# Kernel tuning notes

Hardware: AMD Instinct MI355X
Metric: run time of the kernel (lower is better)

## Reference

```python
import jax, jax.numpy as jnp
import numpy as np

BLOCK_LEN = 64

def _segsum(x):
    """x: (..., T) -> (..., T, T) with segment sums on/below diagonal, -inf above."""
    T = x.shape[-1]
    cs = jnp.cumsum(x, axis=-1)
    seg = cs[..., :, None] - cs[..., None, :]
    mask = jnp.tril(jnp.ones((T, T), dtype=bool))
    return jnp.where(mask, seg, -jnp.inf)

def setup_inputs() -> dict:
    key = jax.random.key(0)
    kX, kA, kB, kC = jax.random.split(key, 4)
    B, S, H, P, N = 2, 4096, 32, 64, 64
    X = jax.random.normal(kX, (B, S, H, P), dtype=jnp.float32)
    # negative decay rates keep exp(cumsum) bounded (real Mamba2 uses A<0)
    A = -jnp.abs(jax.random.normal(kA, (B, S, H), dtype=jnp.float32)) * 0.1
    Bm = jax.random.normal(kB, (B, S, H, N), dtype=jnp.float32)
    Cm = jax.random.normal(kC, (B, S, H, N), dtype=jnp.float32)
    return {"X": X, "A": A, "Bm": Bm, "Cm": Cm}

def reference(X, A, Bm, Cm):
    b, s, h, p = X.shape
    n = Bm.shape[-1]
    l = BLOCK_LEN
    c = s // l
    Xb = X.reshape(b, c, l, h, p)
    Bb = Bm.reshape(b, c, l, h, n)
    Cb = Cm.reshape(b, c, l, h, n)
    Ab = A.reshape(b, c, l, h).transpose(0, 3, 1, 2)  # (b,h,c,l)

    # intra-chunk decay matrix L = exp(segsum(A))  (b,h,c,l,l)
    L = jnp.exp(_segsum(Ab))
    Y_diag = jnp.einsum('bclhn,bcshn,bhcls,bcshp->bclhp', Cb, Bb, L, Xb)

    A_cumsum = jnp.cumsum(Ab, axis=-1)  # (b,h,c,l)
    decay_states = jnp.exp(A_cumsum[..., :, -1:] - A_cumsum)
    states = jnp.einsum('bclhn,bhcl,bclhp->bchpn', Bb, decay_states, Xb)

    init = jnp.zeros_like(states[:, :1])
    states = jnp.concatenate([init, states], axis=1)  # (b,c+1,h,p,n)

    chunk_last = jnp.pad(A_cumsum[..., -1], ((0, 0), (0, 0), (1, 0)))  # (b,h,c+1)
    decay_chunk = jnp.exp(_segsum(chunk_last))  # (b,h,c+1,c+1)
    new_states = jnp.einsum('bhzc,bchpn->bzhpn', decay_chunk, states)
    states = new_states[:, :-1]  # (b,c,h,p,n)

    state_decay_out = jnp.exp(A_cumsum)
    Y_off = jnp.einsum('bclhn,bchpn,bhcl->bclhp', Cb, states, state_decay_out)

    Y = (Y_diag + Y_off).reshape(b, s, h, p)
    return Y
```

## Files before the change

### kernel.cpp

```cpp
#include <hip/hip_runtime.h>
#include <hip/hip_bf16.h>

#define B_ 2
#define S_ 4096
#define H_ 32
#define P_ 64
#define N_ 64
#define C_ 64
#define HP 2048
#define HN 2048

__device__ __forceinline__ float bf2f(unsigned int u16) {
    return __uint_as_float(u16 << 16);
}
__device__ __forceinline__ void unpack2(unsigned int u, float& lo, float& hi) {
    lo = __uint_as_float(u << 16);
    hi = __uint_as_float(u & 0xffff0000u);
}
__device__ __forceinline__ unsigned short f2bf(float f) {
    unsigned int u = __float_as_uint(f);
    u += 0x7fffu + ((u >> 16) & 1u);
    return (unsigned short)(u >> 16);
}

__global__ void k0_detect(const unsigned short* __restrict__ Au, int* __restrict__ flag)
{
    int tid = threadIdx.x;
    unsigned short u = Au[tid * 2];
    int positive = ((u & 0x8000u) == 0) ? 1 : 0;
    unsigned long long m = __ballot(positive);
    if (tid == 0) *flag = (__popcll(m) > 8) ? 1 : 0;
}

__global__ __launch_bounds__(256) void k1_states(
    const void* __restrict__ Xg,
    const void* __restrict__ Ag,
    const void* __restrict__ Bg,
    float* __restrict__ states,
    float* __restrict__ sums,
    const int* __restrict__ flag)
{
    __shared__ __align__(16) float Xs[64][68];
    __shared__ __align__(16) float BwT[64][68];
    __shared__ float wdec[64];

    const int tid = threadIdx.x;
    const int bid = blockIdx.x;
    const int h = bid & 31;
    const int c = (bid >> 5) & 63;
    const int b = bid >> 11;
    const int isf32 = *flag;

    if (tid < 64) {
        int ai = (b * S_ + c * 64 + tid) * H_ + h;
        float a = isf32 ? ((const float*)Ag)[ai] : bf2f(((const unsigned short*)Ag)[ai]);
        float x = a;
        #pragma unroll
        for (int off = 1; off < 64; off <<= 1) {
            float y = __shfl_up(x, off, 64);
            if (tid >= off) x += y;
        }
        float tot = __shfl(x, 63, 64);
        wdec[tid] = __expf(tot - x);
        if (tid == 63) sums[(b * H_ + h) * C_ + c] = tot;
    }
    __syncthreads();

    const size_t baseX = (size_t)((b * S_ + c * 64) * H_ + h) * P_;
    const size_t baseB = (size_t)((b * S_ + c * 64) * H_ + h) * N_;

    if (!isf32) {
        const unsigned short* Xp = (const unsigned short*)Xg + baseX;
        const unsigned short* Bp = (const unsigned short*)Bg + baseB;
        #pragma unroll
        for (int it = 0; it < 2; ++it) {
            int f = it * 2048 + tid * 8;
            int t = f >> 6;
            int e = f & 63;
            uint4 rx = *(const uint4*)(Xp + (size_t)t * HP + e);
            float v0,v1,v2,v3,v4,v5,v6,v7;
            unpack2(rx.x, v0, v1); unpack2(rx.y, v2, v3);
            unpack2(rx.z, v4, v5); unpack2(rx.w, v6, v7);
            float* xr = &Xs[t][e];
            xr[0]=v0; xr[1]=v1; xr[2]=v2; xr[3]=v3; xr[4]=v4; xr[5]=v5; xr[6]=v6; xr[7]=v7;

            uint4 rb = *(const uint4*)(Bp + (size_t)t * HN + e);
            float w = wdec[t];
            unpack2(rb.x, v0, v1); unpack2(rb.y, v2, v3);
            unpack2(rb.z, v4, v5); unpack2(rb.w, v6, v7);
            BwT[e+0][t]=v0*w; BwT[e+1][t]=v1*w; BwT[e+2][t]=v2*w; BwT[e+3][t]=v3*w;
            BwT[e+4][t]=v4*w; BwT[e+5][t]=v5*w; BwT[e+6][t]=v6*w; BwT[e+7][t]=v7*w;
        }
    } else {
        const float* Xp = (const float*)Xg + baseX;
        const float* Bp = (const float*)Bg + baseB;
        #pragma unroll
        for (int it = 0; it < 2; ++it) {
            int f = it * 2048 + tid * 8;
            int t = f >> 6;
            int e = f & 63;
            float4 x0 = *(const float4*)(Xp + (size_t)t * HP + e);
            float4 x1 = *(const float4*)(Xp + (size_t)t * HP + e + 4);
            float* xr = &Xs[t][e];
            xr[0]=x0.x; xr[1]=x0.y; xr[2]=x0.z; xr[3]=x0.w;
            xr[4]=x1.x; xr[5]=x1.y; xr[6]=x1.z; xr[7]=x1.w;

            float4 b0 = *(const float4*)(Bp + (size_t)t * HN + e);
            float4 b1 = *(const float4*)(Bp + (size_t)t * HN + e + 4);
            float w = wdec[t];
            BwT[e+0][t]=b0.x*w; BwT[e+1][t]=b0.y*w; BwT[e+2][t]=b0.z*w; BwT[e+3][t]=b0.w*w;
            BwT[e+4][t]=b1.x*w; BwT[e+5][t]=b1.y*w; BwT[e+6][t]=b1.z*w; BwT[e+7][t]=b1.w*w;
        }
    }
    __syncthreads();

    const int tr = tid >> 4, tc = tid & 15;
    float acc[4][4];
    #pragma unroll
    for (int i = 0; i < 4; ++i)
        #pragma unroll
        for (int j = 0; j < 4; ++j) acc[i][j] = 0.f;

    #pragma unroll 4
    for (int k4 = 0; k4 < 16; ++k4) {
        float la[4][4];
        #pragma unroll
        for (int i = 0; i < 4; ++i) {
            float4 v = *(const float4*)&BwT[tr * 4 + i][k4 * 4];
            la[i][0]=v.x; la[i][1]=v.y; la[i][2]=v.z; la[i][3]=v.w;
        }
        #pragma unroll
        for (int kk = 0; kk < 4; ++kk) {
            float4 r = *(const float4*)&Xs[k4 * 4 + kk][tc * 4];
            #pragma unroll
            for (int i = 0; i < 4; ++i) {
                acc[i][0] += la[i][kk] * r.x;
                acc[i][1] += la[i][kk] * r.y;
                acc[i][2] += la[i][kk] * r.z;
                acc[i][3] += la[i][kk] * r.w;
            }
        }
    }

    float* sp = states + (size_t)((b * C_ + c) * H_ + h) * 4096;
    #pragma unroll
    for (int i = 0; i < 4; ++i) {
        float4 v; v.x=acc[i][0]; v.y=acc[i][1]; v.z=acc[i][2]; v.w=acc[i][3];
        *(float4*)&sp[(tr * 4 + i) * 64 + tc * 4] = v;
    }
}

__global__ __launch_bounds__(256) void k2_scan(
    float* __restrict__ states, const float* __restrict__ sums)
{
    const int tid = threadIdx.x;
    const int bid = blockIdx.x;
    const int split = bid & 3;
    const int bh = bid >> 2;
    const int h = bh & 31;
    const int b = bh >> 5;
    const int e = split * 1024 + tid * 4;
    const float* sm = sums + (b * H_ + h) * C_;
    float4 S; S.x=0.f; S.y=0.f; S.z=0.f; S.w=0.f;
    for (int c = 0; c < 64; ++c) {
        float* p = states + (size_t)((b * C_ + c) * H_ + h) * 4096 + e;
        float4 st = *(const float4*)p;
        *(float4*)p = S;
        float d = __expf(sm[c]);
        S.x = S.x * d + st.x;
        S.y = S.y * d + st.y;
        S.z = S.z * d + st.z;
        S.w = S.w * d + st.w;
    }
}

__global__ __launch_bounds__(256) void k3_y(
    const void* __restrict__ Xg,
    const void* __restrict__ Ag,
    const void* __restrict__ Bg,
    const void* __restrict__ Cg,
    const float* __restrict__ states,
    void* __restrict__ Yg,
    const int* __restrict__ flag)
{
    __shared__ __align__(16) float Cs[64][68];
    __shared__ __align__(16) float Mb[64][68];
    __shared__ __align__(16) float Rb[64][68];
    __shared__ float cs[64];

    const int tid = threadIdx.x;
    const int bid = blockIdx.x;
    const int h = bid & 31;
    const int c = (bid >> 5) & 63;
    const int b = bid >> 11;
    const int isf32 = *flag;

    if (tid < 64) {
        int ai = (b * S_ + c * 64 + tid) * H_ + h;
        float a = isf32 ? ((const float*)Ag)[ai] : bf2f(((const unsigned short*)Ag)[ai]);
        float x = a;
        #pragma unroll
        for (int off = 1; off < 64; off <<= 1) {
            float y = __shfl_up(x, off, 64);
            if (tid >= off) x += y;
        }
        cs[tid] = x;
    }

    const size_t baseX = (size_t)((b * S_ + c * 64) * H_ + h) * P_;
    const size_t baseN = (size_t)((b * S_ + c * 64) * H_ + h) * N_;

    if (!isf32) {
        const unsigned short* Bp = (const unsigned short*)Bg + baseN;
        const unsigned short* Cp = (const unsigned short*)Cg + baseN;
        #pragma unroll
        for (int it = 0; it < 2; ++it) {
            int f = it * 2048 + tid * 8;
            int t = f >> 6;
            int e = f & 63;
            uint4 rc = *(const uint4*)(Cp + (size_t)t * HN + e);
            float v0,v1,v2,v3,v4,v5,v6,v7;
            unpack2(rc.x, v0, v1); unpack2(rc.y, v2, v3);
            unpack2(rc.z, v4, v5); unpack2(rc.w, v6, v7);
            float* cr = &Cs[t][e];
            cr[0]=v0; cr[1]=v1; cr[2]=v2; cr[3]=v3; cr[4]=v4; cr[5]=v5; cr[6]=v6; cr[7]=v7;

            uint4 rb = *(const uint4*)(Bp + (size_t)t * HN + e);
            unpack2(rb.x, v0, v1); unpack2(rb.y, v2, v3);
            unpack2(rb.z, v4, v5); unpack2(rb.w, v6, v7);
            Rb[e+0][t]=v0; Rb[e+1][t]=v1; Rb[e+2][t]=v2; Rb[e+3][t]=v3;
            Rb[e+4][t]=v4; Rb[e+5][t]=v5; Rb[e+6][t]=v6; Rb[e+7][t]=v7;
        }
    } else {
        const float* Bp = (const float*)Bg + baseN;
        const float* Cp = (const float*)Cg + baseN;
        #pragma unroll
        for (int it = 0; it < 2; ++it) {
            int f = it * 2048 + tid * 8;
            int t = f >> 6;
            int e = f & 63;
            float4 c0 = *(const float4*)(Cp + (size_t)t * HN + e);
            float4 c1 = *(const float4*)(Cp + (size_t)t * HN + e + 4);
            float* cr = &Cs[t][e];
            cr[0]=c0.x; cr[1]=c0.y; cr[2]=c0.z; cr[3]=c0.w;
            cr[4]=c1.x; cr[5]=c1.y; cr[6]=c1.z; cr[7]=c1.w;

            float4 b0 = *(const float4*)(Bp + (size_t)t * HN + e);
            float4 b1 = *(const float4*)(Bp + (size_t)t * HN + e + 4);
            Rb[e+0][t]=b0.x; Rb[e+1][t]=b0.y; Rb[e+2][t]=b0.z; Rb[e+3][t]=b0.w;
            Rb[e+4][t]=b1.x; Rb[e+5][t]=b1.y; Rb[e+6][t]=b1.z; Rb[e+7][t]=b1.w;
        }
    }
    __syncthreads();

    const int tr = tid >> 4, tc = tid & 15;

    {
        float acc[4][4];
        #pragma unroll
        for (int i = 0; i < 4; ++i)
            #pragma unroll
            for (int j = 0; j < 4; ++j) acc[i][j] = 0.f;

        #pragma unroll 4
        for (int k4 = 0; k4 < 16; ++k4) {
            float la[4][4];
            #pragma unroll
            for (int i = 0; i < 4; ++i) {
                float4 v = *(const float4*)&Cs[tr * 4 + i][k4 * 4];
                la[i][0]=v.x; la[i][1]=v.y; la[i][2]=v.z; la[i][3]=v.w;
            }
            #pragma unroll
            for (int kk = 0; kk < 4; ++kk) {
                float4 r = *(const float4*)&Rb[k4 * 4 + kk][tc * 4];
                #pragma unroll
                for (int i = 0; i < 4; ++i) {
                    acc[i][0] += la[i][kk] * r.x;
                    acc[i][1] += la[i][kk] * r.y;
                    acc[i][2] += la[i][kk] * r.z;
                    acc[i][3] += la[i][kk] * r.w;
                }
            }
        }

        float ct[4], csj[4];
        #pragma unroll
        for (int i = 0; i < 4; ++i) ct[i] = cs[tr * 4 + i];
        #pragma unroll
        for (int j = 0; j < 4; ++j) csj[j] = cs[tc * 4 + j];
        #pragma unroll
        for (int i = 0; i < 4; ++i) {
            int t = tr * 4 + i;
            float4 mv;
            mv.x = (tc*4+0 <= t) ? acc[i][0] * __expf(ct[i]-csj[0]) : 0.f;
            mv.y = (tc*4+1 <= t) ? acc[i][1] * __expf(ct[i]-csj[1]) : 0.f;
            mv.z = (tc*4+2 <= t) ? acc[i][2] * __expf(ct[i]-csj[2]) : 0.f;
            mv.w = (tc*4+3 <= t) ? acc[i][3] * __expf(ct[i]-csj[3]) : 0.f;
            *(float4*)&Mb[t][tc * 4] = mv;
        }
    }
    __syncthreads();

    if (!isf32) {
        const unsigned short* Xp = (const unsigned short*)Xg + baseX;
        #pragma unroll
        for (int it = 0; it < 2; ++it) {
            int f = it * 2048 + tid * 8;
            int t = f >> 6;
            int e = f & 63;
            uint4 rx = *(const uint4*)(Xp + (size_t)t * HP + e);
            float v0,v1,v2,v3,v4,v5,v6,v7;
            unpack2(rx.x, v0, v1); unpack2(rx.y, v2, v3);
            unpack2(rx.z, v4, v5); unpack2(rx.w, v6, v7);
            float* xr = &Rb[t][e];
            xr[0]=v0; xr[1]=v1; xr[2]=v2; xr[3]=v3; xr[4]=v4; xr[5]=v5; xr[6]=v6; xr[7]=v7;
        }
    } else {
        const float* Xp = (const float*)Xg + baseX;
        #pragma unroll
        for (int it = 0; it < 2; ++it) {
            int f = it * 2048 + tid * 8;
            int t = f >> 6;
            int e = f & 63;
            float4 x0 = *(const float4*)(Xp + (size_t)t * HP + e);
            float4 x1 = *(const float4*)(Xp + (size_t)t * HP + e + 4);
            float* xr = &Rb[t][e];
            xr[0]=x0.x; xr[1]=x0.y; xr[2]=x0.z; xr[3]=x0.w;
            xr[4]=x1.x; xr[5]=x1.y; xr[6]=x1.z; xr[7]=x1.w;
        }
    }
    __syncthreads();

    float accD[4][4];
    #pragma unroll
    for (int i = 0; i < 4; ++i)
        #pragma unroll
        for (int j = 0; j < 4; ++j) accD[i][j] = 0.f;

    #pragma unroll 4
    for (int k4 = 0; k4 < 16; ++k4) {
        float la[4][4];
        #pragma unroll
        for (int i = 0; i < 4; ++i) {
            float4 v = *(const float4*)&Mb[tr * 4 + i][k4 * 4];
            la[i][0]=v.x; la[i][1]=v.y; la[i][2]=v.z; la[i][3]=v.w;
        }
        #pragma unroll
        for (int kk = 0; kk < 4; ++kk) {
            float4 r = *(const float4*)&Rb[k4 * 4 + kk][tc * 4];
            #pragma unroll
            for (int i = 0; i < 4; ++i) {
                accD[i][0] += la[i][kk] * r.x;
                accD[i][1] += la[i][kk] * r.y;
                accD[i][2] += la[i][kk] * r.z;
                accD[i][3] += la[i][kk] * r.w;
            }
        }
    }
    __syncthreads();

    {
        const float* sb = states + (size_t)((b * C_ + c) * H_ + h) * 4096;
        #pragma unroll
        for (int k = 0; k < 4; ++k) {
            int e2 = (k * 256 + tid) * 4;
            float4 v = *(const float4*)(sb + e2);
            *(float4*)&Rb[e2 >> 6][e2 & 63] = v;
        }
    }
    __syncthreads();

    float accO[4][4];
    #pragma unroll
    for (int i = 0; i < 4; ++i)
        #pragma unroll
        for (int j = 0; j < 4; ++j) accO[i][j] = 0.f;

    #pragma unroll 4
    for (int k4 = 0; k4 < 16; ++k4) {
        float la[4][4];
        #pragma unroll
        for (int i = 0; i < 4; ++i) {
            float4 v = *(const float4*)&Cs[tr * 4 + i][k4 * 4];
            la[i][0]=v.x; la[i][1]=v.y; la[i][2]=v.z; la[i][3]=v.w;
        }
        #pragma unroll
        for (int kk = 0; kk < 4; ++kk) {
            float4 r = *(const float4*)&Rb[k4 * 4 + kk][tc * 4];
            #pragma unroll
            for (int i = 0; i < 4; ++i) {
                accO[i][0] += la[i][kk] * r.x;
                accO[i][1] += la[i][kk] * r.y;
                accO[i][2] += la[i][kk] * r.z;
                accO[i][3] += la[i][kk] * r.w;
            }
        }
    }

    if (!isf32) {
        unsigned short* Yp = (unsigned short*)Yg + baseX;
        #pragma unroll
        for (int i = 0; i < 4; ++i) {
            int t = tr * 4 + i;
            float g = __expf(cs[t]);
            ushort4 o;
            o.x = f2bf(accD[i][0] + g * accO[i][0]);
            o.y = f2bf(accD[i][1] + g * accO[i][1]);
            o.z = f2bf(accD[i][2] + g * accO[i][2]);
            o.w = f2bf(accD[i][3] + g * accO[i][3]);
            *(ushort4*)(Yp + (size_t)t * HP + tc * 4) = o;
        }
    } else {
        float* Yp = (float*)Yg + baseX;
        #pragma unroll
        for (int i = 0; i < 4; ++i) {
            int t = tr * 4 + i;
            float g = __expf(cs[t]);
            float4 o;
            o.x = accD[i][0] + g * accO[i][0];
            o.y = accD[i][1] + g * accO[i][1];
            o.z = accD[i][2] + g * accO[i][2];
            o.w = accD[i][3] + g * accO[i][3];
            *(float4*)(Yp + (size_t)t * HP + tc * 4) = o;
        }
    }
}

extern "C" void kernel_launch(void* const* d_in, const int* in_sizes, int n_in,
                              void* d_out, int out_size, void* d_ws, size_t ws_size,
                              hipStream_t stream) {
    const void* X  = d_in[0];
    const void* A  = d_in[1];
    const void* Bm = d_in[2];
    const void* Cm = d_in[3];

    int*   flag   = (int*)d_ws;
    float* sums   = (float*)d_ws + 16;
    float* states = (float*)d_ws + 16 + 4096;

    k0_detect<<<dim3(1), dim3(64), 0, stream>>>((const unsigned short*)A, flag);
    k1_states<<<dim3(B_ * C_ * H_), dim3(256), 0, stream>>>(X, A, Bm, states, sums, flag);
    k2_scan  <<<dim3(B_ * H_ * 4),  dim3(256), 0, stream>>>(states, sums);
    k3_y     <<<dim3(B_ * C_ * H_), dim3(256), 0, stream>>>(X, A, Bm, Cm, states, d_out, flag);
}
```

Baseline: 334.1 us.

## Add bf16 MFMA paths for state and output kernels; widen scan parallelism

Splits the state and output kernels into separate bf16 and fp32 variants, each selected at runtime by the dtype flag. The bf16 variants use 16x16x32 bf16 MFMA instructions with XOR-swizzled LDS tiles and compute intra-chunk and inter-chunk outputs as matrix products. The scan kernel now uses 8 splits per head with float2 elements and prefetches the next chunk's state, for more blocks and more latency hiding. With fp32 inputs only the fp32 variants do real work. The bf16 kernels are still launched and exit early, which adds launch overhead.

```diff
diff --git a/kernel.cpp b/kernel.cpp
--- a/kernel.cpp
+++ b/kernel.cpp
@@ -1,5 +1,4 @@
 #include <hip/hip_runtime.h>
-#include <hip/hip_bf16.h>
 
 #define B_ 2
 #define S_ 4096
@@ -10,6 +9,9 @@
 #define HP 2048
 #define HN 2048
 
+typedef __attribute__((ext_vector_type(8))) short bf16x8;
+typedef __attribute__((ext_vector_type(4))) float f32x4;
+
 __device__ __forceinline__ float bf2f(unsigned int u16) {
     return __uint_as_float(u16 << 16);
 }
@@ -21,6 +23,13 @@
     unsigned int u = __float_as_uint(f);
     u += 0x7fffu + ((u >> 16) & 1u);
     return (unsigned short)(u >> 16);
+}
+
+__device__ __forceinline__ int nsw(int r, int cb) {
+    return (r << 7) + (cb ^ ((r & 7) << 4));
+}
+__device__ __forceinline__ int tsw(int r, int cb) {
+    return (r << 7) + (cb ^ ((((r & 7) ^ (r >> 3)) & 7) << 4));
 }
 
 __global__ void k0_detect(const unsigned short* __restrict__ Au, int* __restrict__ flag)
@@ -32,7 +41,103 @@
     if (tid == 0) *flag = (__popcll(m) > 8) ? 1 : 0;
 }
 
-__global__ __launch_bounds__(256) void k1_states(
+__global__ __launch_bounds__(256) void k1b(
+    const unsigned short* __restrict__ Xg,
+    const unsigned short* __restrict__ Ag,
+    const unsigned short* __restrict__ Bg,
+    float* __restrict__ states,
+    float* __restrict__ sums,
+    const int* __restrict__ flag)
+{
+    if (*flag) return;
+    __shared__ __align__(16) unsigned short XT[64 * 64];
+    __shared__ __align__(16) unsigned short BT[64 * 64];
+    __shared__ float wdec[64];
+
+    const int tid = threadIdx.x;
+    const int bid = blockIdx.x;
+    const int h = bid & 31, c = (bid >> 5) & 63, b = bid >> 11;
+
+    if (tid < 64) {
+        int ai = (b * S_ + c * 64 + tid) * H_ + h;
+        float a = bf2f(Ag[ai]);
+        float x = a;
+        #pragma unroll
+        for (int off = 1; off < 64; off <<= 1) {
+            float y = __shfl_up(x, off, 64);
+            if (tid >= off) x += y;
+        }
+        float tot = __shfl(x, 63, 64);
+        wdec[tid] = __expf(tot - x);
+        if (tid == 63) sums[(b * H_ + h) * C_ + c] = tot;
+    }
+    __syncthreads();
+
+    const size_t baseX = (size_t)((b * S_ + c * 64) * H_ + h) * P_;
+    const size_t baseB = (size_t)((b * S_ + c * 64) * H_ + h) * N_;
+    const unsigned short* Xp = Xg + baseX;
+    const unsigned short* Bp = Bg + baseB;
+    char* XTb = (char*)XT;
+    char* BTb = (char*)BT;
+
+    #pragma unroll
+    for (int it = 0; it < 2; ++it) {
+        int t = (tid >> 3) + it * 32;
+        int e = (tid & 7) * 8;
+        uint4 rx = *(const uint4*)(Xp + (size_t)t * HP + e);
+        const unsigned short* xs = (const unsigned short*)&rx;
+        #pragma unroll
+        for (int i = 0; i < 8; ++i)
+            *(unsigned short*)(XTb + tsw(e + i, 2 * t)) = xs[i];
+
+        uint4 rb = *(const uint4*)(Bp + (size_t)t * HN + e);
+        float w = wdec[t];
+        float v0, v1, v2, v3, v4, v5, v6, v7;
+        unpack2(rb.x, v0, v1); unpack2(rb.y, v2, v3);
+        unpack2(rb.z, v4, v5); unpack2(rb.w, v6, v7);
+        unsigned short bs0 = f2bf(v0 * w), bs1 = f2bf(v1 * w);
+        unsigned short bs2 = f2bf(v2 * w), bs3 = f2bf(v3 * w);
+        unsigned short bs4 = f2bf(v4 * w), bs5 = f2bf(v5 * w);
+        unsigned short bs6 = f2bf(v6 * w), bs7 = f2bf(v7 * w);
+        *(unsigned short*)(BTb + tsw(e + 0, 2 * t)) = bs0;
+        *(unsigned short*)(BTb + tsw(e + 1, 2 * t)) = bs1;
+        *(unsigned short*)(BTb + tsw(e + 2, 2 * t)) = bs2;
+        *(unsigned short*)(BTb + tsw(e + 3, 2 * t)) = bs3;
+        *(unsigned short*)(BTb + tsw(e + 4, 2 * t)) = bs4;
+        *(unsigned short*)(BTb + tsw(e + 5, 2 * t)) = bs5;
+        *(unsigned short*)(BTb + tsw(e + 6, 2 * t)) = bs6;
+        *(unsigned short*)(BTb + tsw(e + 7, 2 * t)) = bs7;
+    }
+    __syncthreads();
+
+    const int l = tid & 63, w4 = tid >> 6;
+    const int lr = l & 15, q = l >> 4;
+
+    bf16x8 a0 = *(const bf16x8*)(XTb + tsw(16 * w4 + lr, 16 * q));
+    bf16x8 a1 = *(const bf16x8*)(XTb + tsw(16 * w4 + lr, 16 * q + 64));
+    f32x4 acc[4];
+    #pragma unroll
+    for (int nt = 0; nt < 4; ++nt) acc[nt] = (f32x4){0.f, 0.f, 0.f, 0.f};
+    #pragma unroll
+    for (int nt = 0; nt < 4; ++nt) {
+        bf16x8 b0 = *(const bf16x8*)(BTb + tsw(16 * nt + lr, 16 * q));
+        acc[nt] = __builtin_amdgcn_mfma_f32_16x16x32_bf16(a0, b0, acc[nt], 0, 0, 0);
+        bf16x8 b1 = *(const bf16x8*)(BTb + tsw(16 * nt + lr, 16 * q + 64));
+        acc[nt] = __builtin_amdgcn_mfma_f32_16x16x32_bf16(a1, b1, acc[nt], 0, 0, 0);
+    }
+
+    float* sp = states + (size_t)((b * C_ + c) * H_ + h) * 4096;
+    #pragma unroll
+    for (int nt = 0; nt < 4; ++nt)
+        #pragma unroll
+        for (int r = 0; r < 4; ++r) {
+            int p = 16 * w4 + 4 * q + r;
+            int n = 16 * nt + lr;
+            sp[p * 64 + n] = acc[nt][r];
+        }
+}
+
+__global__ __launch_bounds__(256) void k1f(
     const void* __restrict__ Xg,
     const void* __restrict__ Ag,
     const void* __restrict__ Bg,
@@ -40,6 +145,7 @@
     float* __restrict__ sums,
     const int* __restrict__ flag)
 {
+    if (!(*flag)) return;
     __shared__ __align__(16) float Xs[64][68];
     __shared__ __align__(16) float BwT[64][68];
     __shared__ float wdec[64];
@@ -49,11 +155,10 @@
     const int h = bid & 31;
     const int c = (bid >> 5) & 63;
     const int b = bid >> 11;
-    const int isf32 = *flag;
 
     if (tid < 64) {
         int ai = (b * S_ + c * 64 + tid) * H_ + h;
-        float a = isf32 ? ((const float*)Ag)[ai] : bf2f(((const unsigned short*)Ag)[ai]);
+        float a = ((const float*)Ag)[ai];
         float x = a;
         #pragma unroll
         for (int off = 1; off < 64; off <<= 1) {
@@ -69,29 +174,7 @@
     const size_t baseX = (size_t)((b * S_ + c * 64) * H_ + h) * P_;
     const size_t baseB = (size_t)((b * S_ + c * 64) * H_ + h) * N_;
 
-    if (!isf32) {
-        const unsigned short* Xp = (const unsigned short*)Xg + baseX;
-        const unsigned short* Bp = (const unsigned short*)Bg + baseB;
-        #pragma unroll
-        for (int it = 0; it < 2; ++it) {
-            int f = it * 2048 + tid * 8;
-            int t = f >> 6;
-            int e = f & 63;
-            uint4 rx = *(const uint4*)(Xp + (size_t)t * HP + e);
-            float v0,v1,v2,v3,v4,v5,v6,v7;
-            unpack2(rx.x, v0, v1); unpack2(rx.y, v2, v3);
-            unpack2(rx.z, v4, v5); unpack2(rx.w, v6, v7);
-            float* xr = &Xs[t][e];
-            xr[0]=v0; xr[1]=v1; xr[2]=v2; xr[3]=v3; xr[4]=v4; xr[5]=v5; xr[6]=v6; xr[7]=v7;
-
-            uint4 rb = *(const uint4*)(Bp + (size_t)t * HN + e);
-            float w = wdec[t];
-            unpack2(rb.x, v0, v1); unpack2(rb.y, v2, v3);
-            unpack2(rb.z, v4, v5); unpack2(rb.w, v6, v7);
-            BwT[e+0][t]=v0*w; BwT[e+1][t]=v1*w; BwT[e+2][t]=v2*w; BwT[e+3][t]=v3*w;
-            BwT[e+4][t]=v4*w; BwT[e+5][t]=v5*w; BwT[e+6][t]=v6*w; BwT[e+7][t]=v7*w;
-        }
-    } else {
+    {
         const float* Xp = (const float*)Xg + baseX;
         const float* Bp = (const float*)Bg + baseB;
         #pragma unroll
@@ -155,26 +238,171 @@
 {
     const int tid = threadIdx.x;
     const int bid = blockIdx.x;
-    const int split = bid & 3;
-    const int bh = bid >> 2;
+    const int split = bid & 7;
+    const int bh = bid >> 3;
     const int h = bh & 31;
     const int b = bh >> 5;
-    const int e = split * 1024 + tid * 4;
+    const int e = split * 512 + tid * 2;
     const float* sm = sums + (b * H_ + h) * C_;
-    float4 S; S.x=0.f; S.y=0.f; S.z=0.f; S.w=0.f;
+    const size_t cstride = (size_t)H_ * 4096;
+    float* p = states + ((size_t)(b * C_) * H_ + h) * 4096 + e;
+    float2 S = make_float2(0.f, 0.f);
+    float2 st = *(const float2*)p;
+    #pragma unroll 4
     for (int c = 0; c < 64; ++c) {
-        float* p = states + (size_t)((b * C_ + c) * H_ + h) * 4096 + e;
-        float4 st = *(const float4*)p;
-        *(float4*)p = S;
+        float2 stn = make_float2(0.f, 0.f);
+        if (c < 63) stn = *(const float2*)(p + cstride);
         float d = __expf(sm[c]);
+        *(float2*)p = S;
         S.x = S.x * d + st.x;
         S.y = S.y * d + st.y;
-        S.z = S.z * d + st.z;
-        S.w = S.w * d + st.w;
-    }
-}
-
-__global__ __launch_bounds__(256) void k3_y(
+        st = stn;
+        p += cstride;
+    }
+}
+
+__global__ __launch_bounds__(256) void k3b(
+    const unsigned short* __restrict__ Xg,
+    const unsigned short* __restrict__ Ag,
+    const unsigned short* __restrict__ Bg,
+    const unsigned short* __restrict__ Cg,
+    const float* __restrict__ states,
+    unsigned short* __restrict__ Yg,
+    const int* __restrict__ flag)
+{
+    if (*flag) return;
+    __shared__ __align__(16) unsigned short Cs[64 * 64];
+    __shared__ __align__(16) unsigned short Bs[64 * 64];
+    __shared__ __align__(16) unsigned short XT[64 * 64];
+    __shared__ __align__(16) unsigned short Ss[64 * 64];
+    __shared__ float csh[64];
+
+    const int tid = threadIdx.x;
+    const int bid = blockIdx.x;
+    const int h = bid & 31, c = (bid >> 5) & 63, b = bid >> 11;
+
+    if (tid < 64) {
+        int ai = (b * S_ + c * 64 + tid) * H_ + h;
+        float a = bf2f(Ag[ai]);
+        float x = a;
+        #pragma unroll
+        for (int off = 1; off < 64; off <<= 1) {
+            float y = __shfl_up(x, off, 64);
+            if (tid >= off) x += y;
+        }
+        csh[tid] = x;
+    }
+
+    const size_t baseX = (size_t)((b * S_ + c * 64) * H_ + h) * P_;
+    const size_t baseN = (size_t)((b * S_ + c * 64) * H_ + h) * N_;
+    const unsigned short* Xp = Xg + baseX;
+    const unsigned short* Bp = Bg + baseN;
+    const unsigned short* Cp = Cg + baseN;
+    char* Csb = (char*)Cs;
+    char* Bsb = (char*)Bs;
+    char* XTb = (char*)XT;
+    char* Ssb = (char*)Ss;
+
+    #pragma unroll
+    for (int it = 0; it < 2; ++it) {
+        int t = (tid >> 3) + it * 32;
+        int e = (tid & 7) * 8;
+        uint4 rc = *(const uint4*)(Cp + (size_t)t * HN + e);
+        *(uint4*)(Csb + nsw(t, 2 * e)) = rc;
+        uint4 rb = *(const uint4*)(Bp + (size_t)t * HN + e);
+        *(uint4*)(Bsb + nsw(t, 2 * e)) = rb;
+        uint4 rx = *(const uint4*)(Xp + (size_t)t * HP + e);
+        const unsigned short* xs = (const unsigned short*)&rx;
+        #pragma unroll
+        for (int i = 0; i < 8; ++i)
+            *(unsigned short*)(XTb + tsw(e + i, 2 * t)) = xs[i];
+    }
+    {
+        const float* sb = states + (size_t)((b * C_ + c) * H_ + h) * 4096;
+        #pragma unroll
+        for (int k = 0; k < 4; ++k) {
+            int e2 = (k * 256 + tid) * 4;
+            float4 v = *(const float4*)(sb + e2);
+            uint2 u;
+            u.x = (unsigned int)f2bf(v.x) | ((unsigned int)f2bf(v.y) << 16);
+            u.y = (unsigned int)f2bf(v.z) | ((unsigned int)f2bf(v.w) << 16);
+            *(uint2*)(Ssb + nsw(e2 >> 6, 2 * (e2 & 63))) = u;
+        }
+    }
+    __syncthreads();
+
+    const int l = tid & 63, w4 = tid >> 6;
+    const int lr = l & 15, q = l >> 4;
+    const int tA = 16 * w4 + lr;
+
+    bf16x8 ac0 = *(const bf16x8*)(Csb + nsw(tA, 16 * q));
+    bf16x8 ac1 = *(const bf16x8*)(Csb + nsw(tA, 16 * q + 64));
+
+    f32x4 mac[4];
+    #pragma unroll
+    for (int st = 0; st < 4; ++st) mac[st] = (f32x4){0.f, 0.f, 0.f, 0.f};
+    #pragma unroll
+    for (int st = 0; st < 4; ++st) {
+        bf16x8 b0 = *(const bf16x8*)(Bsb + nsw(16 * st + lr, 16 * q));
+        mac[st] = __builtin_amdgcn_mfma_f32_16x16x32_bf16(ac0, b0, mac[st], 0, 0, 0);
+        bf16x8 b1 = *(const bf16x8*)(Bsb + nsw(16 * st + lr, 16 * q + 64));
+        mac[st] = __builtin_amdgcn_mfma_f32_16x16x32_bf16(ac1, b1, mac[st], 0, 0, 0);
+    }
+    __syncthreads();
+
+    #pragma unroll
+    for (int st = 0; st < 4; ++st) {
+        int s = 16 * st + lr;
+        float cs_s = csh[s];
+        #pragma unroll
+        for (int r = 0; r < 4; ++r) {
+            int t = 16 * w4 + 4 * q + r;
+            float v = (s <= t) ? mac[st][r] * __expf(csh[t] - cs_s) : 0.f;
+            *(unsigned short*)(Bsb + nsw(t, 2 * s)) = f2bf(v);
+        }
+    }
+    __syncthreads();
+
+    f32x4 yac[4];
+    #pragma unroll
+    for (int pt = 0; pt < 4; ++pt) yac[pt] = (f32x4){0.f, 0.f, 0.f, 0.f};
+
+    bf16x8 am0 = *(const bf16x8*)(Bsb + nsw(tA, 16 * q));
+    bf16x8 am1 = *(const bf16x8*)(Bsb + nsw(tA, 16 * q + 64));
+    #pragma unroll
+    for (int pt = 0; pt < 4; ++pt) {
+        bf16x8 x0 = *(const bf16x8*)(XTb + tsw(16 * pt + lr, 16 * q));
+        yac[pt] = __builtin_amdgcn_mfma_f32_16x16x32_bf16(am0, x0, yac[pt], 0, 0, 0);
+        bf16x8 x1 = *(const bf16x8*)(XTb + tsw(16 * pt + lr, 16 * q + 64));
+        yac[pt] = __builtin_amdgcn_mfma_f32_16x16x32_bf16(am1, x1, yac[pt], 0, 0, 0);
+    }
+
+    float g = __expf(csh[tA]);
+    bf16x8 as0, as1;
+    #pragma unroll
+    for (int i = 0; i < 8; ++i) {
+        as0[i] = (short)f2bf(bf2f((unsigned short)ac0[i]) * g);
+        as1[i] = (short)f2bf(bf2f((unsigned short)ac1[i]) * g);
+    }
+    #pragma unroll
+    for (int pt = 0; pt < 4; ++pt) {
+        bf16x8 s0 = *(const bf16x8*)(Ssb + nsw(16 * pt + lr, 16 * q));
+        yac[pt] = __builtin_amdgcn_mfma_f32_16x16x32_bf16(as0, s0, yac[pt], 0, 0, 0);
+        bf16x8 s1 = *(const bf16x8*)(Ssb + nsw(16 * pt + lr, 16 * q + 64));
+        yac[pt] = __builtin_amdgcn_mfma_f32_16x16x32_bf16(as1, s1, yac[pt], 0, 0, 0);
+    }
+
+    unsigned short* Yp = Yg + baseX;
+    #pragma unroll
+    for (int pt = 0; pt < 4; ++pt)
+        #pragma unroll
+        for (int r = 0; r < 4; ++r) {
+            int t = 16 * w4 + 4 * q + r;
+            Yp[(size_t)t * HP + 16 * pt + lr] = f2bf(yac[pt][r]);
+        }
+}
+
+__global__ __launch_bounds__(256) void k3f(
     const void* __restrict__ Xg,
     const void* __restrict__ Ag,
     const void* __restrict__ Bg,
@@ -183,6 +411,7 @@
     void* __restrict__ Yg,
     const int* __restrict__ flag)
 {
+    if (!(*flag)) return;
     __shared__ __align__(16) float Cs[64][68];
     __shared__ __align__(16) float Mb[64][68];
     __shared__ __align__(16) float Rb[64][68];
@@ -193,11 +422,10 @@
     const int h = bid & 31;
     const int c = (bid >> 5) & 63;
     const int b = bid >> 11;
-    const int isf32 = *flag;
 
     if (tid < 64) {
         int ai = (b * S_ + c * 64 + tid) * H_ + h;
-        float a = isf32 ? ((const float*)Ag)[ai] : bf2f(((const unsigned short*)Ag)[ai]);
+        float a = ((const float*)Ag)[ai];
         float x = a;
         #pragma unroll
         for (int off = 1; off < 64; off <<= 1) {
@@ -210,28 +438,7 @@
     const size_t baseX = (size_t)((b * S_ + c * 64) * H_ + h) * P_;
     const size_t baseN = (size_t)((b * S_ + c * 64) * H_ + h) * N_;
 
-    if (!isf32) {
-        const unsigned short* Bp = (const unsigned short*)Bg + baseN;
-        const unsigned short* Cp = (const unsigned short*)Cg + baseN;
-        #pragma unroll
-        for (int it = 0; it < 2; ++it) {
-            int f = it * 2048 + tid * 8;
-            int t = f >> 6;
-            int e = f & 63;
-            uint4 rc = *(const uint4*)(Cp + (size_t)t * HN + e);
-            float v0,v1,v2,v3,v4,v5,v6,v7;
-            unpack2(rc.x, v0, v1); unpack2(rc.y, v2, v3);
-            unpack2(rc.z, v4, v5); unpack2(rc.w, v6, v7);
-            float* cr = &Cs[t][e];
-            cr[0]=v0; cr[1]=v1; cr[2]=v2; cr[3]=v3; cr[4]=v4; cr[5]=v5; cr[6]=v6; cr[7]=v7;
-
-            uint4 rb = *(const uint4*)(Bp + (size_t)t * HN + e);
-            unpack2(rb.x, v0, v1); unpack2(rb.y, v2, v3);
-            unpack2(rb.z, v4, v5); unpack2(rb.w, v6, v7);
-            Rb[e+0][t]=v0; Rb[e+1][t]=v1; Rb[e+2][t]=v2; Rb[e+3][t]=v3;
-            Rb[e+4][t]=v4; Rb[e+5][t]=v5; Rb[e+6][t]=v6; Rb[e+7][t]=v7;
-        }
-    } else {
+    {
         const float* Bp = (const float*)Bg + baseN;
         const float* Cp = (const float*)Cg + baseN;
         #pragma unroll
@@ -301,21 +508,7 @@
     }
     __syncthreads();
 
-    if (!isf32) {
-        const unsigned short* Xp = (const unsigned short*)Xg + baseX;
-        #pragma unroll
-        for (int it = 0; it < 2; ++it) {
-            int f = it * 2048 + tid * 8;
-            int t = f >> 6;
-            int e = f & 63;
-            uint4 rx = *(const uint4*)(Xp + (size_t)t * HP + e);
-            float v0,v1,v2,v3,v4,v5,v6,v7;
-            unpack2(rx.x, v0, v1); unpack2(rx.y, v2, v3);
-            unpack2(rx.z, v4, v5); unpack2(rx.w, v6, v7);
-            float* xr = &Rb[t][e];
-            xr[0]=v0; xr[1]=v1; xr[2]=v2; xr[3]=v3; xr[4]=v4; xr[5]=v5; xr[6]=v6; xr[7]=v7;
-        }
-    } else {
+    {
         const float* Xp = (const float*)Xg + baseX;
         #pragma unroll
         for (int it = 0; it < 2; ++it) {
@@ -397,20 +590,7 @@
         }
     }
 
-    if (!isf32) {
-        unsigned short* Yp = (unsigned short*)Yg + baseX;
-        #pragma unroll
-        for (int i = 0; i < 4; ++i) {
-            int t = tr * 4 + i;
-            float g = __expf(cs[t]);
-            ushort4 o;
-            o.x = f2bf(accD[i][0] + g * accO[i][0]);
-            o.y = f2bf(accD[i][1] + g * accO[i][1]);
-            o.z = f2bf(accD[i][2] + g * accO[i][2]);
-            o.w = f2bf(accD[i][3] + g * accO[i][3]);
-            *(ushort4*)(Yp + (size_t)t * HP + tc * 4) = o;
-        }
-    } else {
+    {
         float* Yp = (float*)Yg + baseX;
         #pragma unroll
         for (int i = 0; i < 4; ++i) {
@@ -421,7 +601,7 @@
             o.y = accD[i][1] + g * accO[i][1];
             o.z = accD[i][2] + g * accO[i][2];
             o.w = accD[i][3] + g * accO[i][3];
-            *(float4*)(Yp + (size_t)t * HP + tc * 4) = o;
+            *(float4*)&Yp[(size_t)t * HP + tc * 4] = o;
         }
     }
 }
@@ -439,7 +619,14 @@
     float* states = (float*)d_ws + 16 + 4096;
 
     k0_detect<<<dim3(1), dim3(64), 0, stream>>>((const unsigned short*)A, flag);
-    k1_states<<<dim3(B_ * C_ * H_), dim3(256), 0, stream>>>(X, A, Bm, states, sums, flag);
-    k2_scan  <<<dim3(B_ * H_ * 4),  dim3(256), 0, stream>>>(states, sums);
-    k3_y     <<<dim3(B_ * C_ * H_), dim3(256), 0, stream>>>(X, A, Bm, Cm, states, d_out, flag);
-}
+    k1b<<<dim3(B_ * C_ * H_), dim3(256), 0, stream>>>(
+        (const unsigned short*)X, (const unsigned short*)A,
+        (const unsigned short*)Bm, states, sums, flag);
+    k1f<<<dim3(B_ * C_ * H_), dim3(256), 0, stream>>>(X, A, Bm, states, sums, flag);
+    k2_scan<<<dim3(B_ * H_ * 8), dim3(256), 0, stream>>>(states, sums);
+    k3b<<<dim3(B_ * C_ * H_), dim3(256), 0, stream>>>(
+        (const unsigned short*)X, (const unsigned short*)A,
+        (const unsigned short*)Bm, (const unsigned short*)Cm,
+        states, (unsigned short*)d_out, flag);
+    k3f<<<dim3(B_ * C_ * H_), dim3(256), 0, stream>>>(X, A, Bm, Cm, states, d_out, flag);
+}
```

After: 337.8 us. Within noise of the previous version (+1.1%).
